# Optimization experiments

Measured on AMD Instinct MI355X. Metric: run time of the kernel, lower is better.

The kernel has to match this reference:

```python
import jax, jax.numpy as jnp
import numpy as np

N = 100000
E = 640000
F_IN, F_HID, F_OUT = 128, 128, 40
EPS = 1e-5


def setup_inputs() -> dict:
    key = jax.random.key(0)
    ks = jax.random.split(key, 12)
    d = {
        "x": jax.random.normal(ks[0], (N, F_IN), dtype=jnp.float32),
        "src": jax.random.randint(ks[1], (E,), 0, N, dtype=jnp.int32),
        "dst": jax.random.randint(ks[2], (E,), 0, N, dtype=jnp.int32),
        # GCNConv weights (glorot-ish) and biases
        "W1": jax.random.normal(ks[3], (F_IN, F_HID), dtype=jnp.float32) / np.sqrt(F_IN),
        "b1": jnp.zeros((F_HID,), jnp.float32),
        "W2": jax.random.normal(ks[4], (F_HID, F_HID), dtype=jnp.float32) / np.sqrt(F_HID),
        "b2": jnp.zeros((F_HID,), jnp.float32),
        "W3": jax.random.normal(ks[5], (F_HID, F_OUT), dtype=jnp.float32) / np.sqrt(F_HID),
        "b3": jnp.zeros((F_OUT,), jnp.float32),
        # BatchNorm affine params for the two hidden layers
        "g1": jnp.ones((F_HID,), jnp.float32),
        "be1": jnp.zeros((F_HID,), jnp.float32),
        "g2": jnp.ones((F_HID,), jnp.float32),
        "be2": jnp.zeros((F_HID,), jnp.float32),
    }
    return d


def _gcn_norm(src, dst):
    # add self-loops, compute symmetric normalization deg^-1/2 A_hat deg^-1/2
    loops = jnp.arange(N, dtype=src.dtype)
    s = jnp.concatenate([src, loops])
    t = jnp.concatenate([dst, loops])
    deg = jax.ops.segment_sum(jnp.ones_like(t, dtype=jnp.float32), t, num_segments=N)
    dinv = jax.lax.rsqrt(jnp.maximum(deg, 1.0))
    norm = dinv[s] * dinv[t]  # [E+N]
    return s, t, norm


def _conv(x, W, b, s, t, norm):
    h = x @ W                                  # [N, Fout]
    msg = h[s] * norm[:, None]                 # [E+N, Fout] gather
    out = jax.ops.segment_sum(msg, t, num_segments=N)  # scatter-add
    return out + b


def _bn(x, g, b):
    # BatchNorm1d over the node dimension (batch statistics, eval dropout=0)
    mu = jnp.mean(x, axis=0)
    var = jnp.var(x, axis=0)
    return (x - mu) * jax.lax.rsqrt(var + EPS) * g + b


def reference(x, src, dst, W1, b1, W2, b2, W3, b3, g1, be1, g2, be2):
    s, t, norm = _gcn_norm(src, dst)
    h = jax.nn.relu(_bn(_conv(x, W1, b1, s, t, norm), g1, be1))
    h = jax.nn.relu(_bn(_conv(h, W2, b2, s, t, norm), g2, be2))
    h = _conv(h, W3, b3, s, t, norm)
    return jax.nn.log_softmax(h, axis=-1)
```

## Files before the change

### kernel.cpp

```cpp
#include <hip/hip_runtime.h>
#include <cstdint>
#include <cstddef>

#define FEAT 128
#define FOUT 40
constexpr float BN_EPS = 1e-5f;

typedef __attribute__((ext_vector_type(8))) short bf16x8;
typedef __attribute__((ext_vector_type(4))) float f32x4;

__device__ __forceinline__ unsigned short f2bf(float f) {
    unsigned u = __float_as_uint(f);
    u += 0x7FFFu + ((u >> 16) & 1u);
    return (unsigned short)(u >> 16);
}
__device__ __forceinline__ float bflo(unsigned u) { return __uint_as_float(u << 16); }
__device__ __forceinline__ float bfhi(unsigned u) { return __uint_as_float(u & 0xFFFF0000u); }
__device__ __forceinline__ unsigned packbf2(float a, float b) {
    return (unsigned)f2bf(a) | ((unsigned)f2bf(b) << 16);
}


__global__ __launch_bounds__(256) void count_k(const int* __restrict__ dst, int* __restrict__ cnt, int E) {
    int e = blockIdx.x * 256 + threadIdx.x;
    if (e < E) atomicAdd(&cnt[dst[e]], 1);
}

__global__ __launch_bounds__(256) void scan1_k(const int* __restrict__ cnt, int* __restrict__ bsum, int n) {
    __shared__ int sh[256];
    int base = blockIdx.x * 1024, t = threadIdx.x;
    int s = 0;
#pragma unroll
    for (int j = 0; j < 4; ++j) {
        int idx = base + t * 4 + j;
        if (idx < n) s += cnt[idx];
    }
    sh[t] = s;
    __syncthreads();
    for (int o = 128; o > 0; o >>= 1) {
        if (t < o) sh[t] += sh[t + o];
        __syncthreads();
    }
    if (t == 0) bsum[blockIdx.x] = sh[0];
}

__global__ void scan2_k(const int* __restrict__ bsum, int* __restrict__ boff, int nb,
                        int* __restrict__ offs, int n, int E) {
    __shared__ int sh[256];
    int t = threadIdx.x;
    if (nb <= 256) {
        int v = (t < nb) ? bsum[t] : 0;
        sh[t] = v;
        __syncthreads();
        for (int o = 1; o < 256; o <<= 1) {
            int x = (t >= o) ? sh[t - o] : 0;
            __syncthreads();
            sh[t] += x;
            __syncthreads();
        }
        if (t < nb) boff[t] = sh[t] - v;
        if (t == 0) offs[n] = E;
    } else if (t == 0) {
        int run = 0;
        for (int i = 0; i < nb; ++i) { boff[i] = run; run += bsum[i]; }
        offs[n] = E;
    }
}

__global__ __launch_bounds__(256) void scan3_k(const int* __restrict__ cnt, const int* __restrict__ boff,
                                               int* __restrict__ offs, int* __restrict__ cursor,
                                               float* __restrict__ dinv, int n) {
    __shared__ int sh[256];
    int base = blockIdx.x * 1024, t = threadIdx.x;
    int c[4];
    int s = 0;
#pragma unroll
    for (int j = 0; j < 4; ++j) {
        int idx = base + t * 4 + j;
        c[j] = (idx < n) ? cnt[idx] : 0;
        s += c[j];
    }
    sh[t] = s;
    __syncthreads();
    for (int o = 1; o < 256; o <<= 1) {
        int v = (t >= o) ? sh[t - o] : 0;
        __syncthreads();
        sh[t] += v;
        __syncthreads();
    }
    int g = boff[blockIdx.x] + sh[t] - s;
#pragma unroll
    for (int j = 0; j < 4; ++j) {
        int idx = base + t * 4 + j;
        if (idx < n) {
            offs[idx] = g;
            cursor[idx] = g;
            dinv[idx] = rsqrtf((float)(c[j] + 1));
        }
        g += c[j];
    }
}

__global__ __launch_bounds__(256) void fill_k(const int* __restrict__ src, const int* __restrict__ dst,
                                              int* __restrict__ cursor, int* __restrict__ csr, int E) {
    int e = blockIdx.x * 256 + threadIdx.x;
    if (e < E) {
        int d = dst[e];
        int p = atomicAdd(&cursor[d], 1);
        csr[p] = src[e];
    }
}


__global__ __launch_bounds__(256) void castW_k(const float* __restrict__ W1, const float* __restrict__ W2,
                                               const float* __restrict__ W3,
                                               unsigned short* __restrict__ Wt1, unsigned short* __restrict__ Wt2,
                                               unsigned short* __restrict__ Wt3) {
    int tid = blockIdx.x * 256 + threadIdx.x;
    int stride = gridDim.x * 256;
    for (int i = tid; i < 4 * 4 * 128 * 8; i += stride) {
        int j = i & 7, c = (i >> 3) & 127, q = (i >> 10) & 3, kt = i >> 12;
        int k = kt * 32 + q * 8 + j;
        Wt1[i] = f2bf(W1[k * 128 + c]);
        Wt2[i] = f2bf(W2[k * 128 + c]);
    }
    for (int i = tid; i < 4 * 4 * 48 * 8; i += stride) {
        int j = i & 7, rest = i >> 3;
        int c = rest % 48, kq = rest / 48;
        int q = kq & 3, kt = kq >> 2;
        int k = kt * 32 + q * 8 + j;
        Wt3[i] = (c < FOUT) ? f2bf(W3[k * FOUT + c]) : (unsigned short)0;
    }
}


template <int SRC>
__global__ __launch_bounds__(256, 3) void gemm128_k(const void* __restrict__ srcp,
                                                    const unsigned short* __restrict__ Wt,
                                                    const float* __restrict__ ss,
                                                    const float* __restrict__ dinv,
                                                    unsigned short* __restrict__ Hb,
                                                    int ntiles, int nreal) {
    __shared__ uint4 XsU[64 * 16];
    unsigned short* Xs = (unsigned short*)XsU;

    const int t = threadIdx.x;
    const int tc = t & 15;
    const int l = t & 63, w = t >> 6;
    const int wm = w >> 1, wn = w & 1;
    const int lr = l & 15, q = l >> 4;

    float sc[8], sh[8];
    if (SRC == 1) {
#pragma unroll
        for (int j = 0; j < 8; ++j) { sc[j] = ss[tc * 8 + j]; sh[j] = ss[128 + tc * 8 + j]; }
    }

    bf16x8 Bf[4][4];
#pragma unroll
    for (int kt = 0; kt < 4; ++kt)
#pragma unroll
        for (int n = 0; n < 4; ++n) {
            int col = wn * 64 + n * 16 + lr;
            Bf[kt][n] = *(const bf16x8*)&((const uint4*)Wt)[(kt * 4 + q) * 128 + col];
        }

    for (int tile = blockIdx.x; tile < ntiles; tile += gridDim.x) {
        const int row0 = tile * 64;
        __syncthreads();
#pragma unroll
        for (int k2 = 0; k2 < 4; ++k2) {
            int row = (t >> 4) + k2 * 16;
            int grow = row0 + row;
            uint4 o;
            if (SRC == 0) {
                if (grow < nreal) {
                    const float4* xp = (const float4*)((const float*)srcp + (size_t)grow * FEAT + tc * 8);
                    float4 f0 = xp[0], f1 = xp[1];
                    o.x = packbf2(f0.x, f0.y); o.y = packbf2(f0.z, f0.w);
                    o.z = packbf2(f1.x, f1.y); o.w = packbf2(f1.z, f1.w);
                } else {
                    o.x = 0u; o.y = 0u; o.z = 0u; o.w = 0u;
                }
            } else {
                uint4 u = ((const uint4*)((const unsigned short*)srcp + (size_t)grow * FEAT))[tc];
                float v0 = fmaxf(fmaf(bflo(u.x), sc[0], sh[0]), 0.f);
                float v1 = fmaxf(fmaf(bfhi(u.x), sc[1], sh[1]), 0.f);
                float v2 = fmaxf(fmaf(bflo(u.y), sc[2], sh[2]), 0.f);
                float v3 = fmaxf(fmaf(bfhi(u.y), sc[3], sh[3]), 0.f);
                float v4 = fmaxf(fmaf(bflo(u.z), sc[4], sh[4]), 0.f);
                float v5 = fmaxf(fmaf(bfhi(u.z), sc[5], sh[5]), 0.f);
                float v6 = fmaxf(fmaf(bflo(u.w), sc[6], sh[6]), 0.f);
                float v7 = fmaxf(fmaf(bfhi(u.w), sc[7], sh[7]), 0.f);
                o.x = packbf2(v0, v1); o.y = packbf2(v2, v3);
                o.z = packbf2(v4, v5); o.w = packbf2(v6, v7);
            }
            XsU[row * 16 + (tc ^ (row & 7))] = o;
        }
        __syncthreads();

        f32x4 acc[2][4];
#pragma unroll
        for (int m = 0; m < 2; ++m)
#pragma unroll
            for (int n = 0; n < 4; ++n)
#pragma unroll
                for (int r2 = 0; r2 < 4; ++r2) acc[m][n][r2] = 0.f;

#pragma unroll
        for (int kt = 0; kt < 4; ++kt) {
            int rowA = wm * 32 + lr;
            bf16x8 A0 = *(const bf16x8*)&XsU[rowA * 16 + ((kt * 4 + q) ^ (rowA & 7))];
            int rowB = rowA + 16;
            bf16x8 A1 = *(const bf16x8*)&XsU[rowB * 16 + ((kt * 4 + q) ^ (rowB & 7))];
#pragma unroll
            for (int n = 0; n < 4; ++n) {
                acc[0][n] = __builtin_amdgcn_mfma_f32_16x16x32_bf16(A0, Bf[kt][n], acc[0][n], 0, 0, 0);
                acc[1][n] = __builtin_amdgcn_mfma_f32_16x16x32_bf16(A1, Bf[kt][n], acc[1][n], 0, 0, 0);
            }
        }
        __syncthreads();

#pragma unroll
        for (int m = 0; m < 2; ++m) {
            float dv[4];
#pragma unroll
            for (int r = 0; r < 4; ++r) dv[r] = dinv[row0 + wm * 32 + m * 16 + q * 4 + r];
#pragma unroll
            for (int n = 0; n < 4; ++n) {
                int col = wn * 64 + n * 16 + lr;
#pragma unroll
                for (int r = 0; r < 4; ++r) {
                    int row = wm * 32 + m * 16 + q * 4 + r;
                    Xs[row * 128 + (((col >> 3) ^ (row & 7)) << 3) + (col & 7)] = f2bf(acc[m][n][r] * dv[r]);
                }
            }
        }
        __syncthreads();
#pragma unroll
        for (int k2 = 0; k2 < 4; ++k2) {
            int row = (t >> 4) + k2 * 16;
            ((uint4*)&Hb[(size_t)(row0 + row) * FEAT])[tc] = XsU[row * 16 + (tc ^ (row & 7))];
        }
    }
}


__global__ __launch_bounds__(256, 4) void gemm40_k(const unsigned short* __restrict__ srcp,
                                                   const unsigned short* __restrict__ Wt,
                                                   const float* __restrict__ ss,
                                                   const float* __restrict__ dinv,
                                                   unsigned short* __restrict__ H3,
                                                   int ntiles) {
    __shared__ uint4 XsU[64 * 16];
    unsigned short* Xs = (unsigned short*)XsU;
    const int t = threadIdx.x, tc = t & 15;
    const int l = t & 63, w = t >> 6, lr = l & 15, q = l >> 4;

    float sc[8], sh[8];
#pragma unroll
    for (int j = 0; j < 8; ++j) { sc[j] = ss[tc * 8 + j]; sh[j] = ss[128 + tc * 8 + j]; }

    bf16x8 Bf[4][3];
#pragma unroll
    for (int kt = 0; kt < 4; ++kt)
#pragma unroll
        for (int n = 0; n < 3; ++n)
            Bf[kt][n] = *(const bf16x8*)&((const uint4*)Wt)[(kt * 4 + q) * 48 + n * 16 + lr];

    for (int tile = blockIdx.x; tile < ntiles; tile += gridDim.x) {
        const int row0 = tile * 64;
        __syncthreads();
#pragma unroll
        for (int k2 = 0; k2 < 4; ++k2) {
            int row = (t >> 4) + k2 * 16;
            int grow = row0 + row;
            uint4 u = ((const uint4*)(srcp + (size_t)grow * FEAT))[tc];
            float v0 = fmaxf(fmaf(bflo(u.x), sc[0], sh[0]), 0.f);
            float v1 = fmaxf(fmaf(bfhi(u.x), sc[1], sh[1]), 0.f);
            float v2 = fmaxf(fmaf(bflo(u.y), sc[2], sh[2]), 0.f);
            float v3 = fmaxf(fmaf(bfhi(u.y), sc[3], sh[3]), 0.f);
            float v4 = fmaxf(fmaf(bflo(u.z), sc[4], sh[4]), 0.f);
            float v5 = fmaxf(fmaf(bfhi(u.z), sc[5], sh[5]), 0.f);
            float v6 = fmaxf(fmaf(bflo(u.w), sc[6], sh[6]), 0.f);
            float v7 = fmaxf(fmaf(bfhi(u.w), sc[7], sh[7]), 0.f);
            uint4 o;
            o.x = packbf2(v0, v1); o.y = packbf2(v2, v3);
            o.z = packbf2(v4, v5); o.w = packbf2(v6, v7);
            XsU[row * 16 + (tc ^ (row & 7))] = o;
        }
        __syncthreads();

        f32x4 acc[3];
#pragma unroll
        for (int n = 0; n < 3; ++n)
#pragma unroll
            for (int r2 = 0; r2 < 4; ++r2) acc[n][r2] = 0.f;

#pragma unroll
        for (int kt = 0; kt < 4; ++kt) {
            int row = w * 16 + lr;
            bf16x8 A = *(const bf16x8*)&XsU[row * 16 + ((kt * 4 + q) ^ (row & 7))];
#pragma unroll
            for (int n = 0; n < 3; ++n)
                acc[n] = __builtin_amdgcn_mfma_f32_16x16x32_bf16(A, Bf[kt][n], acc[n], 0, 0, 0);
        }
        __syncthreads();

        float dv[4];
#pragma unroll
        for (int r = 0; r < 4; ++r) dv[r] = dinv[row0 + w * 16 + q * 4 + r];
#pragma unroll
        for (int n = 0; n < 3; ++n) {
            int col = n * 16 + lr;
#pragma unroll
            for (int r = 0; r < 4; ++r) {
                int row = w * 16 + q * 4 + r;
                Xs[row * 128 + (((col >> 3) ^ (row & 7)) << 3) + (col & 7)] = f2bf(acc[n][r] * dv[r]);
            }
        }
        __syncthreads();
        for (int i = t; i < 384; i += 256) {
            int row = i / 6, cc = i - row * 6;
            ((uint4*)&H3[(size_t)(row0 + row) * 64])[cc] = XsU[row * 16 + (cc ^ (row & 7))];
        }
    }
}


__global__ __launch_bounds__(256) void agg128_k(const uint4* __restrict__ Hb4, const int* __restrict__ offs,
                                                const int* __restrict__ csr, const float* __restrict__ dinv,
                                                const float* __restrict__ bias, uint4* __restrict__ Zb4,
                                                float* __restrict__ sums, int n) {
    const int t = threadIdx.x;
    const int g16 = t >> 4;
    const int l16 = t & 15;
    float bs[8];
#pragma unroll
    for (int j = 0; j < 8; ++j) bs[j] = bias[l16 * 8 + j];
    float s[8] = {0.f,0.f,0.f,0.f,0.f,0.f,0.f,0.f};
    float qq[8] = {0.f,0.f,0.f,0.f,0.f,0.f,0.f,0.f};

    for (int node = blockIdx.x * 16 + g16; node < n; node += gridDim.x * 16) {
        int beg = offs[node], end = offs[node + 1];
        uint4 u = Hb4[(size_t)node * 16 + l16];
        float a[8];
        a[0] = bflo(u.x); a[1] = bfhi(u.x); a[2] = bflo(u.y); a[3] = bfhi(u.y);
        a[4] = bflo(u.z); a[5] = bfhi(u.z); a[6] = bflo(u.w); a[7] = bfhi(u.w);
        for (int e = beg; e < end; e += 8) {
            int rem = end - e;
            int s0 = csr[e];
            int s1 = (rem > 1) ? csr[e + 1] : s0;
            int s2 = (rem > 2) ? csr[e + 2] : s0;
            int s3 = (rem > 3) ? csr[e + 3] : s0;
            int s4 = (rem > 4) ? csr[e + 4] : s0;
            int s5 = (rem > 5) ? csr[e + 5] : s0;
            int s6 = (rem > 6) ? csr[e + 6] : s0;
            int s7 = (rem > 7) ? csr[e + 7] : s0;
            uint4 v0 = Hb4[(size_t)s0 * 16 + l16];
            uint4 v1 = Hb4[(size_t)s1 * 16 + l16];
            uint4 v2 = Hb4[(size_t)s2 * 16 + l16];
            uint4 v3 = Hb4[(size_t)s3 * 16 + l16];
            uint4 v4 = Hb4[(size_t)s4 * 16 + l16];
            uint4 v5 = Hb4[(size_t)s5 * 16 + l16];
            uint4 v6 = Hb4[(size_t)s6 * 16 + l16];
            uint4 v7 = Hb4[(size_t)s7 * 16 + l16];
#define ACC8(v) { a[0]+=bflo(v.x); a[1]+=bfhi(v.x); a[2]+=bflo(v.y); a[3]+=bfhi(v.y); \
                  a[4]+=bflo(v.z); a[5]+=bfhi(v.z); a[6]+=bflo(v.w); a[7]+=bfhi(v.w); }
            ACC8(v0);
            if (rem > 1) ACC8(v1);
            if (rem > 2) ACC8(v2);
            if (rem > 3) ACC8(v3);
            if (rem > 4) ACC8(v4);
            if (rem > 5) ACC8(v5);
            if (rem > 6) ACC8(v6);
            if (rem > 7) ACC8(v7);
#undef ACC8
        }
        float dv = dinv[node];
        float z[8];
#pragma unroll
        for (int j = 0; j < 8; ++j) {
            z[j] = fmaf(a[j], dv, bs[j]);
            s[j] += z[j];
            qq[j] += z[j] * z[j];
        }
        uint4 o;
        o.x = packbf2(z[0], z[1]); o.y = packbf2(z[2], z[3]);
        o.z = packbf2(z[4], z[5]); o.w = packbf2(z[6], z[7]);
        Zb4[(size_t)node * 16 + l16] = o;
    }

    __shared__ float red[2][16][128];
#pragma unroll
    for (int j = 0; j < 8; ++j) {
        red[0][g16][l16 * 8 + j] = s[j];
        red[1][g16][l16 * 8 + j] = qq[j];
    }
    __syncthreads();
    int f = t & 127, which = t >> 7;
    float acc = 0.f;
#pragma unroll
    for (int G = 0; G < 16; ++G) acc += red[which][G][f];
    atomicAdd(&sums[which * 128 + f], acc);
}

__global__ void bnfinal_k(const float* __restrict__ sums, const float* __restrict__ g,
                          const float* __restrict__ be, float* __restrict__ ss, int n) {
    int c = threadIdx.x;
    float inv_n = 1.0f / (float)n;
    float mu = sums[c] * inv_n;
    float var = sums[128 + c] * inv_n - mu * mu;
    float rstd = rsqrtf(var + BN_EPS);
    float scv = g[c] * rstd;
    ss[c] = scv;
    ss[128 + c] = be[c] - mu * scv;
}


__global__ __launch_bounds__(256) void agg40_k(const uint4* __restrict__ H34, const int* __restrict__ offs,
                                               const int* __restrict__ csr, const float* __restrict__ dinv,
                                               const float* __restrict__ bias, float* __restrict__ out, int n) {
    const int t = threadIdx.x;
    const int g8 = t >> 3, l8 = t & 7;
    float bl[8];
#pragma unroll
    for (int j = 0; j < 8; ++j) {
        int fj = l8 * 8 + j;
        bl[j] = (fj < FOUT) ? bias[fj] : 0.f;
    }

    for (int node = blockIdx.x * 32 + g8; node < n; node += gridDim.x * 32) {
        int beg = offs[node], end = offs[node + 1];
        uint4 u = H34[(size_t)node * 8 + l8];
        float a[8];
        a[0]=bflo(u.x); a[1]=bfhi(u.x); a[2]=bflo(u.y); a[3]=bfhi(u.y);
        a[4]=bflo(u.z); a[5]=bfhi(u.z); a[6]=bflo(u.w); a[7]=bfhi(u.w);

        for (int e = beg; e < end; e += 8) {
            int rem = end - e;
            int s0 = csr[e];
            int s1 = (rem > 1) ? csr[e + 1] : s0;
            int s2 = (rem > 2) ? csr[e + 2] : s0;
            int s3 = (rem > 3) ? csr[e + 3] : s0;
            int s4 = (rem > 4) ? csr[e + 4] : s0;
            int s5 = (rem > 5) ? csr[e + 5] : s0;
            int s6 = (rem > 6) ? csr[e + 6] : s0;
            int s7 = (rem > 7) ? csr[e + 7] : s0;
            uint4 v0 = H34[(size_t)s0 * 8 + l8];
            uint4 v1 = H34[(size_t)s1 * 8 + l8];
            uint4 v2 = H34[(size_t)s2 * 8 + l8];
            uint4 v3 = H34[(size_t)s3 * 8 + l8];
            uint4 v4 = H34[(size_t)s4 * 8 + l8];
            uint4 v5 = H34[(size_t)s5 * 8 + l8];
            uint4 v6 = H34[(size_t)s6 * 8 + l8];
            uint4 v7 = H34[(size_t)s7 * 8 + l8];
#define ACC8(v) { a[0]+=bflo(v.x); a[1]+=bfhi(v.x); a[2]+=bflo(v.y); a[3]+=bfhi(v.y); \
                  a[4]+=bflo(v.z); a[5]+=bfhi(v.z); a[6]+=bflo(v.w); a[7]+=bfhi(v.w); }
            ACC8(v0);
            if (rem > 1) ACC8(v1);
            if (rem > 2) ACC8(v2);
            if (rem > 3) ACC8(v3);
            if (rem > 4) ACC8(v4);
            if (rem > 5) ACC8(v5);
            if (rem > 6) ACC8(v6);
            if (rem > 7) ACC8(v7);
#undef ACC8
        }

        float dv = dinv[node];
        float val[8];
        float m = -INFINITY;
#pragma unroll
        for (int j = 0; j < 8; ++j) {
            int fj = l8 * 8 + j;
            val[j] = (fj < FOUT) ? fmaf(a[j], dv, bl[j]) : -INFINITY;
            m = fmaxf(m, val[j]);
        }
#pragma unroll
        for (int o = 4; o > 0; o >>= 1) m = fmaxf(m, __shfl_xor(m, o, 8));
        float es = 0.f;
#pragma unroll
        for (int j = 0; j < 8; ++j) es += (l8 * 8 + j < FOUT) ? expf(val[j] - m) : 0.f;
#pragma unroll
        for (int o = 4; o > 0; o >>= 1) es += __shfl_xor(es, o, 8);
        float lse = m + logf(es);
        if (l8 < 5) {
            float4 o0 = make_float4(val[0]-lse, val[1]-lse, val[2]-lse, val[3]-lse);
            float4 o1 = make_float4(val[4]-lse, val[5]-lse, val[6]-lse, val[7]-lse);
            float* op = out + (size_t)node * FOUT + l8 * 8;
            *(float4*)op = o0;
            *(float4*)(op + 4) = o1;
        }
    }
}


extern "C" void kernel_launch(void* const* d_in, const int* in_sizes, int n_in,
                              void* d_out, int out_size, void* d_ws, size_t ws_size,
                              hipStream_t stream) {
    const float* x   = (const float*)d_in[0];
    const int*   src = (const int*)d_in[1];
    const int*   dst = (const int*)d_in[2];
    const float* W1  = (const float*)d_in[3];
    const float* b1  = (const float*)d_in[4];
    const float* W2  = (const float*)d_in[5];
    const float* b2  = (const float*)d_in[6];
    const float* W3  = (const float*)d_in[7];
    const float* b3  = (const float*)d_in[8];
    const float* g1  = (const float*)d_in[9];
    const float* be1 = (const float*)d_in[10];
    const float* g2  = (const float*)d_in[11];
    const float* be2 = (const float*)d_in[12];

    const int N = in_sizes[0] / FEAT;
    const int E = in_sizes[1];
    const int Np = (N + 63) & ~63;
    const int ntiles = Np / 64;
    float* out = (float*)d_out;

    char* p = (char*)d_ws;
    auto alloc = [&](size_t bytes) {
        char* r = p;
        p += (bytes + 255) & ~(size_t)255;
        return r;
    };
    float* dinv   = (float*)alloc((size_t)Np * 4);
    int*   cnt    = (int*)alloc((size_t)N * 4);
    int*   offs   = (int*)alloc((size_t)(N + 1) * 4);
    int*   cursor = (int*)alloc((size_t)N * 4);
    int*   csr    = (int*)alloc((size_t)E * 4);
    int*   bsum   = (int*)alloc(1024);
    int*   boff   = (int*)alloc(1024);
    float* sums   = (float*)alloc(1024);
    float* ss     = (float*)alloc(1024);
    unsigned short* Wt1 = (unsigned short*)alloc(4 * 4 * 128 * 8 * 2);
    unsigned short* Wt2 = (unsigned short*)alloc(4 * 4 * 128 * 8 * 2);
    unsigned short* Wt3 = (unsigned short*)alloc(4 * 4 * 48 * 8 * 2);
    unsigned short* Hb  = (unsigned short*)alloc((size_t)Np * FEAT * 2);
    unsigned short* Zb  = (unsigned short*)alloc((size_t)Np * FEAT * 2);
    unsigned short* H3  = (unsigned short*)alloc((size_t)Np * 64 * 2);

    const int nb = (N + 1023) / 1024;
    const int eb = (E + 255) / 256;

    hipMemsetAsync(cnt, 0, (size_t)N * 4, stream);
    count_k<<<eb, 256, 0, stream>>>(dst, cnt, E);
    scan1_k<<<nb, 256, 0, stream>>>(cnt, bsum, N);
    scan2_k<<<1, 256, 0, stream>>>(bsum, boff, nb, offs, N, E);
    scan3_k<<<nb, 256, 0, stream>>>(cnt, boff, offs, cursor, dinv, N);
    fill_k<<<eb, 256, 0, stream>>>(src, dst, cursor, csr, E);
    castW_k<<<48, 256, 0, stream>>>(W1, W2, W3, Wt1, Wt2, Wt3);

    gemm128_k<0><<<768, 256, 0, stream>>>(x, Wt1, nullptr, dinv, Hb, ntiles, N);
    hipMemsetAsync(sums, 0, 1024, stream);
    agg128_k<<<2048, 256, 0, stream>>>((const uint4*)Hb, offs, csr, dinv, b1, (uint4*)Zb, sums, N);
    bnfinal_k<<<1, 128, 0, stream>>>(sums, g1, be1, ss, N);

    gemm128_k<1><<<768, 256, 0, stream>>>(Zb, Wt2, ss, dinv, Hb, ntiles, N);
    hipMemsetAsync(sums, 0, 1024, stream);
    agg128_k<<<2048, 256, 0, stream>>>((const uint4*)Hb, offs, csr, dinv, b2, (uint4*)Zb, sums, N);
    bnfinal_k<<<1, 128, 0, stream>>>(sums, g2, be2, ss, N);

    gemm40_k<<<1024, 256, 0, stream>>>(Zb, Wt3, ss, dinv, H3, ntiles);
    agg40_k<<<2048, 256, 0, stream>>>((const uint4*)H3, offs, csr, dinv, b3, out, N);
}
```

Baseline: 296.6 us.

## Fuse CSR build into one cooperative kernel and fold BN finalize into GEMMs

Replaces the memset plus five CSR-construction launches (count, three scan stages, fill) with a single cooperative kernel that uses grid-wide syncs between phases. It also removes the two bnfinal launches by computing BatchNorm scale and shift inside the following GEMM kernels, and zeroes both stats buffers in the weight-cast kernel instead of with separate memsets. The aim is to cut launch count and inter-kernel gaps. The trade-offs are grid.sync barriers across 1024 blocks and every GEMM thread recomputing the BN statistics.

```diff
diff --git a/kernel.cpp b/kernel.cpp
--- a/kernel.cpp
+++ b/kernel.cpp
@@ -1,6 +1,9 @@
 #include <hip/hip_runtime.h>
+#include <hip/hip_cooperative_groups.h>
 #include <cstdint>
 #include <cstddef>
+
+namespace cg = cooperative_groups;
 
 #define FEAT 128
 #define FOUT 40
@@ -21,90 +24,97 @@
 }
 
 
-__global__ __launch_bounds__(256) void count_k(const int* __restrict__ dst, int* __restrict__ cnt, int E) {
-    int e = blockIdx.x * 256 + threadIdx.x;
-    if (e < E) atomicAdd(&cnt[dst[e]], 1);
-}
-
-__global__ __launch_bounds__(256) void scan1_k(const int* __restrict__ cnt, int* __restrict__ bsum, int n) {
+__global__ __launch_bounds__(256) void csr_build_k(const int* __restrict__ src, const int* __restrict__ dst,
+                                                   int* __restrict__ cnt, int* __restrict__ offs,
+                                                   int* __restrict__ cursor, float* __restrict__ dinv,
+                                                   int* __restrict__ csr, int* __restrict__ bsum,
+                                                   int* __restrict__ boff, int n, int E, int nb) {
+    cg::grid_group grid = cg::this_grid();
     __shared__ int sh[256];
-    int base = blockIdx.x * 1024, t = threadIdx.x;
-    int s = 0;
-#pragma unroll
-    for (int j = 0; j < 4; ++j) {
-        int idx = base + t * 4 + j;
-        if (idx < n) s += cnt[idx];
-    }
-    sh[t] = s;
-    __syncthreads();
-    for (int o = 128; o > 0; o >>= 1) {
-        if (t < o) sh[t] += sh[t + o];
-        __syncthreads();
-    }
-    if (t == 0) bsum[blockIdx.x] = sh[0];
-}
-
-__global__ void scan2_k(const int* __restrict__ bsum, int* __restrict__ boff, int nb,
-                        int* __restrict__ offs, int n, int E) {
-    __shared__ int sh[256];
-    int t = threadIdx.x;
-    if (nb <= 256) {
-        int v = (t < nb) ? bsum[t] : 0;
-        sh[t] = v;
+    const int t = threadIdx.x;
+    const int gtid = blockIdx.x * 256 + t;
+    const int gstride = gridDim.x * 256;
+
+    for (int i = gtid; i < n; i += gstride) cnt[i] = 0;
+    grid.sync();
+
+    for (int e = gtid; e < E; e += gstride) atomicAdd(&cnt[dst[e]], 1);
+    grid.sync();
+
+    for (int chunk = blockIdx.x; chunk < nb; chunk += gridDim.x) {
+        int base = chunk * 1024;
+        int s = 0;
+#pragma unroll
+        for (int j = 0; j < 4; ++j) {
+            int idx = base + t * 4 + j;
+            if (idx < n) s += cnt[idx];
+        }
+        sh[t] = s;
+        __syncthreads();
+        for (int o = 128; o > 0; o >>= 1) {
+            if (t < o) sh[t] += sh[t + o];
+            __syncthreads();
+        }
+        if (t == 0) bsum[chunk] = sh[0];
+        __syncthreads();
+    }
+    grid.sync();
+
+    if (blockIdx.x == 0) {
+        if (nb <= 256) {
+            int v = (t < nb) ? bsum[t] : 0;
+            sh[t] = v;
+            __syncthreads();
+            for (int o = 1; o < 256; o <<= 1) {
+                int x = (t >= o) ? sh[t - o] : 0;
+                __syncthreads();
+                sh[t] += x;
+                __syncthreads();
+            }
+            if (t < nb) boff[t] = sh[t] - v;
+            if (t == 0) offs[n] = E;
+        } else if (t == 0) {
+            int run = 0;
+            for (int i = 0; i < nb; ++i) { boff[i] = run; run += bsum[i]; }
+            offs[n] = E;
+        }
+    }
+    grid.sync();
+
+    for (int chunk = blockIdx.x; chunk < nb; chunk += gridDim.x) {
+        int base = chunk * 1024;
+        int c[4];
+        int s = 0;
+#pragma unroll
+        for (int j = 0; j < 4; ++j) {
+            int idx = base + t * 4 + j;
+            c[j] = (idx < n) ? cnt[idx] : 0;
+            s += c[j];
+        }
+        sh[t] = s;
         __syncthreads();
         for (int o = 1; o < 256; o <<= 1) {
-            int x = (t >= o) ? sh[t - o] : 0;
+            int v = (t >= o) ? sh[t - o] : 0;
             __syncthreads();
-            sh[t] += x;
+            sh[t] += v;
             __syncthreads();
         }
-        if (t < nb) boff[t] = sh[t] - v;
-        if (t == 0) offs[n] = E;
-    } else if (t == 0) {
-        int run = 0;
-        for (int i = 0; i < nb; ++i) { boff[i] = run; run += bsum[i]; }
-        offs[n] = E;
-    }
-}
-
-__global__ __launch_bounds__(256) void scan3_k(const int* __restrict__ cnt, const int* __restrict__ boff,
-                                               int* __restrict__ offs, int* __restrict__ cursor,
-                                               float* __restrict__ dinv, int n) {
-    __shared__ int sh[256];
-    int base = blockIdx.x * 1024, t = threadIdx.x;
-    int c[4];
-    int s = 0;
-#pragma unroll
-    for (int j = 0; j < 4; ++j) {
-        int idx = base + t * 4 + j;
-        c[j] = (idx < n) ? cnt[idx] : 0;
-        s += c[j];
-    }
-    sh[t] = s;
-    __syncthreads();
-    for (int o = 1; o < 256; o <<= 1) {
-        int v = (t >= o) ? sh[t - o] : 0;
-        __syncthreads();
-        sh[t] += v;
-        __syncthreads();
-    }
-    int g = boff[blockIdx.x] + sh[t] - s;
-#pragma unroll
-    for (int j = 0; j < 4; ++j) {
-        int idx = base + t * 4 + j;
-        if (idx < n) {
-            offs[idx] = g;
-            cursor[idx] = g;
-            dinv[idx] = rsqrtf((float)(c[j] + 1));
-        }
-        g += c[j];
-    }
-}
-
-__global__ __launch_bounds__(256) void fill_k(const int* __restrict__ src, const int* __restrict__ dst,
-                                              int* __restrict__ cursor, int* __restrict__ csr, int E) {
-    int e = blockIdx.x * 256 + threadIdx.x;
-    if (e < E) {
+        int g = boff[chunk] + sh[t] - s;
+#pragma unroll
+        for (int j = 0; j < 4; ++j) {
+            int idx = base + t * 4 + j;
+            if (idx < n) {
+                offs[idx] = g;
+                cursor[idx] = g;
+                dinv[idx] = rsqrtf((float)(c[j] + 1));
+            }
+            g += c[j];
+        }
+        __syncthreads();
+    }
+    grid.sync();
+
+    for (int e = gtid; e < E; e += gstride) {
         int d = dst[e];
         int p = atomicAdd(&cursor[d], 1);
         csr[p] = src[e];
@@ -115,9 +125,11 @@
 __global__ __launch_bounds__(256) void castW_k(const float* __restrict__ W1, const float* __restrict__ W2,
                                                const float* __restrict__ W3,
                                                unsigned short* __restrict__ Wt1, unsigned short* __restrict__ Wt2,
-                                               unsigned short* __restrict__ Wt3) {
+                                               unsigned short* __restrict__ Wt3,
+                                               float* __restrict__ sums1, float* __restrict__ sums2) {
     int tid = blockIdx.x * 256 + threadIdx.x;
     int stride = gridDim.x * 256;
+    if (tid < 256) { sums1[tid] = 0.f; sums2[tid] = 0.f; }
     for (int i = tid; i < 4 * 4 * 128 * 8; i += stride) {
         int j = i & 7, c = (i >> 3) & 127, q = (i >> 10) & 3, kt = i >> 12;
         int k = kt * 32 + q * 8 + j;
@@ -137,7 +149,10 @@
 template <int SRC>
 __global__ __launch_bounds__(256, 3) void gemm128_k(const void* __restrict__ srcp,
                                                     const unsigned short* __restrict__ Wt,
-                                                    const float* __restrict__ ss,
+                                                    const float* __restrict__ sums,
+                                                    const float* __restrict__ gam,
+                                                    const float* __restrict__ bet,
+                                                    float inv_n,
                                                     const float* __restrict__ dinv,
                                                     unsigned short* __restrict__ Hb,
                                                     int ntiles, int nreal) {
@@ -150,10 +165,18 @@
     const int wm = w >> 1, wn = w & 1;
     const int lr = l & 15, q = l >> 4;
 
-    float sc[8], sh[8];
+    float sc[8], sh2[8];
     if (SRC == 1) {
 #pragma unroll
-        for (int j = 0; j < 8; ++j) { sc[j] = ss[tc * 8 + j]; sh[j] = ss[128 + tc * 8 + j]; }
+        for (int j = 0; j < 8; ++j) {
+            int f = tc * 8 + j;
+            float mu = sums[f] * inv_n;
+            float var = sums[128 + f] * inv_n - mu * mu;
+            float rstd = rsqrtf(var + BN_EPS);
+            float scv = gam[f] * rstd;
+            sc[j] = scv;
+            sh2[j] = bet[f] - mu * scv;
+        }
     }
 
     bf16x8 Bf[4][4];
@@ -184,14 +207,14 @@
                 }
             } else {
                 uint4 u = ((const uint4*)((const unsigned short*)srcp + (size_t)grow * FEAT))[tc];
-                float v0 = fmaxf(fmaf(bflo(u.x), sc[0], sh[0]), 0.f);
-                float v1 = fmaxf(fmaf(bfhi(u.x), sc[1], sh[1]), 0.f);
-                float v2 = fmaxf(fmaf(bflo(u.y), sc[2], sh[2]), 0.f);
-                float v3 = fmaxf(fmaf(bfhi(u.y), sc[3], sh[3]), 0.f);
-                float v4 = fmaxf(fmaf(bflo(u.z), sc[4], sh[4]), 0.f);
-                float v5 = fmaxf(fmaf(bfhi(u.z), sc[5], sh[5]), 0.f);
-                float v6 = fmaxf(fmaf(bflo(u.w), sc[6], sh[6]), 0.f);
-                float v7 = fmaxf(fmaf(bfhi(u.w), sc[7], sh[7]), 0.f);
+                float v0 = fmaxf(fmaf(bflo(u.x), sc[0], sh2[0]), 0.f);
+                float v1 = fmaxf(fmaf(bfhi(u.x), sc[1], sh2[1]), 0.f);
+                float v2 = fmaxf(fmaf(bflo(u.y), sc[2], sh2[2]), 0.f);
+                float v3 = fmaxf(fmaf(bfhi(u.y), sc[3], sh2[3]), 0.f);
+                float v4 = fmaxf(fmaf(bflo(u.z), sc[4], sh2[4]), 0.f);
+                float v5 = fmaxf(fmaf(bfhi(u.z), sc[5], sh2[5]), 0.f);
+                float v6 = fmaxf(fmaf(bflo(u.w), sc[6], sh2[6]), 0.f);
+                float v7 = fmaxf(fmaf(bfhi(u.w), sc[7], sh2[7]), 0.f);
                 o.x = packbf2(v0, v1); o.y = packbf2(v2, v3);
                 o.z = packbf2(v4, v5); o.w = packbf2(v6, v7);
             }
@@ -248,7 +271,10 @@
 
 __global__ __launch_bounds__(256, 4) void gemm40_k(const unsigned short* __restrict__ srcp,
                                                    const unsigned short* __restrict__ Wt,
-                                                   const float* __restrict__ ss,
+                                                   const float* __restrict__ sums,
+                                                   const float* __restrict__ gam,
+                                                   const float* __restrict__ bet,
+                                                   float inv_n,
                                                    const float* __restrict__ dinv,
                                                    unsigned short* __restrict__ H3,
                                                    int ntiles) {
@@ -257,9 +283,17 @@
     const int t = threadIdx.x, tc = t & 15;
     const int l = t & 63, w = t >> 6, lr = l & 15, q = l >> 4;
 
-    float sc[8], sh[8];
-#pragma unroll
-    for (int j = 0; j < 8; ++j) { sc[j] = ss[tc * 8 + j]; sh[j] = ss[128 + tc * 8 + j]; }
+    float sc[8], sh2[8];
+#pragma unroll
+    for (int j = 0; j < 8; ++j) {
+        int f = tc * 8 + j;
+        float mu = sums[f] * inv_n;
+        float var = sums[128 + f] * inv_n - mu * mu;
+        float rstd = rsqrtf(var + BN_EPS);
+        float scv = gam[f] * rstd;
+        sc[j] = scv;
+        sh2[j] = bet[f] - mu * scv;
+    }
 
     bf16x8 Bf[4][3];
 #pragma unroll
@@ -276,14 +310,14 @@
             int row = (t >> 4) + k2 * 16;
             int grow = row0 + row;
             uint4 u = ((const uint4*)(srcp + (size_t)grow * FEAT))[tc];
-            float v0 = fmaxf(fmaf(bflo(u.x), sc[0], sh[0]), 0.f);
-            float v1 = fmaxf(fmaf(bfhi(u.x), sc[1], sh[1]), 0.f);
-            float v2 = fmaxf(fmaf(bflo(u.y), sc[2], sh[2]), 0.f);
-            float v3 = fmaxf(fmaf(bfhi(u.y), sc[3], sh[3]), 0.f);
-            float v4 = fmaxf(fmaf(bflo(u.z), sc[4], sh[4]), 0.f);
-            float v5 = fmaxf(fmaf(bfhi(u.z), sc[5], sh[5]), 0.f);
-            float v6 = fmaxf(fmaf(bflo(u.w), sc[6], sh[6]), 0.f);
-            float v7 = fmaxf(fmaf(bfhi(u.w), sc[7], sh[7]), 0.f);
+            float v0 = fmaxf(fmaf(bflo(u.x), sc[0], sh2[0]), 0.f);
+            float v1 = fmaxf(fmaf(bfhi(u.x), sc[1], sh2[1]), 0.f);
+            float v2 = fmaxf(fmaf(bflo(u.y), sc[2], sh2[2]), 0.f);
+            float v3 = fmaxf(fmaf(bfhi(u.y), sc[3], sh2[3]), 0.f);
+            float v4 = fmaxf(fmaf(bflo(u.z), sc[4], sh2[4]), 0.f);
+            float v5 = fmaxf(fmaf(bfhi(u.z), sc[5], sh2[5]), 0.f);
+            float v6 = fmaxf(fmaf(bflo(u.w), sc[6], sh2[6]), 0.f);
+            float v7 = fmaxf(fmaf(bfhi(u.w), sc[7], sh2[7]), 0.f);
             uint4 o;
             o.x = packbf2(v0, v1); o.y = packbf2(v2, v3);
             o.z = packbf2(v4, v5); o.w = packbf2(v6, v7);
@@ -405,18 +439,6 @@
     atomicAdd(&sums[which * 128 + f], acc);
 }
 
-__global__ void bnfinal_k(const float* __restrict__ sums, const float* __restrict__ g,
-                          const float* __restrict__ be, float* __restrict__ ss, int n) {
-    int c = threadIdx.x;
-    float inv_n = 1.0f / (float)n;
-    float mu = sums[c] * inv_n;
-    float var = sums[128 + c] * inv_n - mu * mu;
-    float rstd = rsqrtf(var + BN_EPS);
-    float scv = g[c] * rstd;
-    ss[c] = scv;
-    ss[128 + c] = be[c] - mu * scv;
-}
-
 
 __global__ __launch_bounds__(256) void agg40_k(const uint4* __restrict__ H34, const int* __restrict__ offs,
                                                const int* __restrict__ csr, const float* __restrict__ dinv,
@@ -517,6 +539,7 @@
     const int E = in_sizes[1];
     const int Np = (N + 63) & ~63;
     const int ntiles = Np / 64;
+    const float inv_n = 1.0f / (float)N;
     float* out = (float*)d_out;
 
     char* p = (char*)d_ws;
@@ -532,8 +555,8 @@
     int*   csr    = (int*)alloc((size_t)E * 4);
     int*   bsum   = (int*)alloc(1024);
     int*   boff   = (int*)alloc(1024);
-    float* sums   = (float*)alloc(1024);
-    float* ss     = (float*)alloc(1024);
+    float* sums1  = (float*)alloc(1024);
+    float* sums2  = (float*)alloc(1024);
     unsigned short* Wt1 = (unsigned short*)alloc(4 * 4 * 128 * 8 * 2);
     unsigned short* Wt2 = (unsigned short*)alloc(4 * 4 * 128 * 8 * 2);
     unsigned short* Wt3 = (unsigned short*)alloc(4 * 4 * 48 * 8 * 2);
@@ -541,27 +564,24 @@
     unsigned short* Zb  = (unsigned short*)alloc((size_t)Np * FEAT * 2);
     unsigned short* H3  = (unsigned short*)alloc((size_t)Np * 64 * 2);
 
-    const int nb = (N + 1023) / 1024;
-    const int eb = (E + 255) / 256;
-
-    hipMemsetAsync(cnt, 0, (size_t)N * 4, stream);
-    count_k<<<eb, 256, 0, stream>>>(dst, cnt, E);
-    scan1_k<<<nb, 256, 0, stream>>>(cnt, bsum, N);
-    scan2_k<<<1, 256, 0, stream>>>(bsum, boff, nb, offs, N, E);
-    scan3_k<<<nb, 256, 0, stream>>>(cnt, boff, offs, cursor, dinv, N);
-    fill_k<<<eb, 256, 0, stream>>>(src, dst, cursor, csr, E);
-    castW_k<<<48, 256, 0, stream>>>(W1, W2, W3, Wt1, Wt2, Wt3);
-
-    gemm128_k<0><<<768, 256, 0, stream>>>(x, Wt1, nullptr, dinv, Hb, ntiles, N);
-    hipMemsetAsync(sums, 0, 1024, stream);
-    agg128_k<<<2048, 256, 0, stream>>>((const uint4*)Hb, offs, csr, dinv, b1, (uint4*)Zb, sums, N);
-    bnfinal_k<<<1, 128, 0, stream>>>(sums, g1, be1, ss, N);
-
-    gemm128_k<1><<<768, 256, 0, stream>>>(Zb, Wt2, ss, dinv, Hb, ntiles, N);
-    hipMemsetAsync(sums, 0, 1024, stream);
-    agg128_k<<<2048, 256, 0, stream>>>((const uint4*)Hb, offs, csr, dinv, b2, (uint4*)Zb, sums, N);
-    bnfinal_k<<<1, 128, 0, stream>>>(sums, g2, be2, ss, N);
-
-    gemm40_k<<<1024, 256, 0, stream>>>(Zb, Wt3, ss, dinv, H3, ntiles);
+    int nb = (N + 1023) / 1024;
+
+    {
+        const int* srcA = src; const int* dstA = dst;
+        int nA = N, eA = E, nbA = nb;
+        void* args[] = {(void*)&srcA, (void*)&dstA, (void*)&cnt, (void*)&offs, (void*)&cursor,
+                        (void*)&dinv, (void*)&csr, (void*)&bsum, (void*)&boff,
+                        (void*)&nA, (void*)&eA, (void*)&nbA};
+        hipLaunchCooperativeKernel((void*)csr_build_k, dim3(1024), dim3(256), args, 0, stream);
+    }
+    castW_k<<<48, 256, 0, stream>>>(W1, W2, W3, Wt1, Wt2, Wt3, sums1, sums2);
+
+    gemm128_k<0><<<768, 256, 0, stream>>>(x, Wt1, nullptr, nullptr, nullptr, 0.f, dinv, Hb, ntiles, N);
+    agg128_k<<<2048, 256, 0, stream>>>((const uint4*)Hb, offs, csr, dinv, b1, (uint4*)Zb, sums1, N);
+
+    gemm128_k<1><<<768, 256, 0, stream>>>(Zb, Wt2, sums1, g1, be1, inv_n, dinv, Hb, ntiles, N);
+    agg128_k<<<2048, 256, 0, stream>>>((const uint4*)Hb, offs, csr, dinv, b2, (uint4*)Zb, sums2, N);
+
+    gemm40_k<<<1024, 256, 0, stream>>>(Zb, Wt3, sums2, g2, be2, inv_n, dinv, H3, ntiles);
     agg40_k<<<2048, 256, 0, stream>>>((const uint4*)H3, offs, csr, dinv, b3, out, N);
 }
```

New measurement: 761.9 us. 2.57x slower.
